# Optimization experiments

Hardware: AMD Instinct MI355X
Metric: run time of the kernel (lower is better)

The kernel has to match this reference:

```python
import jax, jax.numpy as jnp
import numpy as np

N = 100000      # nodes
E = 1600000     # directed edges (avg degree 16)
DIN, DH, DOUT = 128, 128, 64


def gcn_conv(x, W, b, src, dst, n):
    """PyG GCNConv: out = D^{-1/2} (A + I) D^{-1/2} (x @ W) + b.
    src/dst already include self-loops."""
    deg = jax.ops.segment_sum(jnp.ones_like(src, dtype=x.dtype), dst, num_segments=n)
    dinv = jnp.where(deg > 0, jax.lax.rsqrt(deg), jnp.zeros_like(deg))
    norm = dinv[src] * dinv[dst]                      # [E+N]
    h = x @ W                                         # [N, dout] linear first (PyG)
    msg = h[src] * norm[:, None]                      # gather + scale, [E+N, dout]
    return jax.ops.segment_sum(msg, dst, num_segments=n) + b


def setup_inputs() -> dict:
    key = jax.random.key(0)
    k1, k2, k3 = jax.random.split(key, 3)
    x = jax.random.normal(k1, (N, DIN), dtype=jnp.float32)
    edge_index = jax.random.randint(k2, (2, E), 0, N, dtype=jnp.int64)
    kw1, kw2 = jax.random.split(k3)
    # glorot-style init for the two GCN linear weights
    W1 = jax.random.normal(kw1, (DIN, DH), dtype=jnp.float32) * (1.0 / np.sqrt(DIN))
    b1 = jnp.zeros((DH,), dtype=jnp.float32)
    W2 = jax.random.normal(kw2, (DH, DOUT), dtype=jnp.float32) * (1.0 / np.sqrt(DH))
    b2 = jnp.zeros((DOUT,), dtype=jnp.float32)
    return {"x": x, "W1": W1, "b1": b1, "W2": W2, "b2": b2, "edge_index": edge_index}


def reference(x, W1, b1, W2, b2, edge_index):
    n = x.shape[0]
    loops = jnp.arange(n, dtype=edge_index.dtype)
    src = jnp.concatenate([edge_index[0], loops])     # add self-loops
    dst = jnp.concatenate([edge_index[1], loops])
    h = jax.nn.relu(gcn_conv(x, W1, b1, src, dst, n))
    return gcn_conv(h, W2, b2, src, dst, n)
```

## Files before the change

### kernel.cpp

```cpp
#include <hip/hip_runtime.h>

#define N_NODES 100000
#define N_EDGES 1600000
#define BUCKET_SHIFT 9
#define NB 196
#define BIN_BLOCKS 782
#define GEMM_BLOCKS 1563
#define BCAP 10240
#define AGG1_BLOCKS 6250
#define AGG2_BLOCKS 3125

typedef short bf16x8 __attribute__((ext_vector_type(8)));
typedef float f32x4 __attribute__((ext_vector_type(4)));
typedef float f32x8 __attribute__((ext_vector_type(8)));

__device__ __forceinline__ unsigned short f2bf(float f) {
    unsigned int u = __float_as_uint(f);
    unsigned int r = (u + 0x7FFFu + ((u >> 16) & 1u)) >> 16;
    return (unsigned short)r;
}
__device__ __forceinline__ float bf2f(unsigned short b) {
    return __uint_as_float(((unsigned int)b) << 16);
}
__device__ __forceinline__ void acc8(float* a, uint4 v) {
    a[0] += __uint_as_float(v.x << 16);
    a[1] += __uint_as_float(v.x & 0xFFFF0000u);
    a[2] += __uint_as_float(v.y << 16);
    a[3] += __uint_as_float(v.y & 0xFFFF0000u);
    a[4] += __uint_as_float(v.z << 16);
    a[5] += __uint_as_float(v.z & 0xFFFF0000u);
    a[6] += __uint_as_float(v.w << 16);
    a[7] += __uint_as_float(v.w & 0xFFFF0000u);
}

__global__ __launch_bounds__(256) void k_tw(const float* __restrict__ W1, const float* __restrict__ W2,
                                            unsigned short* __restrict__ w1t, unsigned short* __restrict__ w2t,
                                            int* __restrict__ bcur) {
    int t = blockIdx.x * 256 + threadIdx.x;
    if (t < 16384) {
        int k = t >> 7, c = t & 127;
        w1t[c * 128 + k] = f2bf(W1[t]);
    } else if (t < 24576) {
        int i = t - 16384;
        int k = i >> 6, c = i & 63;
        w2t[c * 128 + k] = f2bf(W2[i]);
    } else if (t - 24576 < NB) {
        bcur[t - 24576] = 0;
    }
}

__global__ __launch_bounds__(256) void k_bin(const int* __restrict__ src, const int* __restrict__ dst,
                                             int* __restrict__ bcur, int* __restrict__ ebuf) {
    __shared__ int hist[NB];
    __shared__ int lbase[NB];
    int t = threadIdx.x;
    int e0 = blockIdx.x * 2048 + t;
    int s[8], d[8];
#pragma unroll
    for (int j = 0; j < 8; ++j) {
        int e = e0 + j * 256;
        bool ok = e < N_EDGES;
        s[j] = ok ? src[e] : -1;
        d[j] = ok ? dst[e] : 0;
    }
    if (t < NB) hist[t] = 0;
    __syncthreads();
#pragma unroll
    for (int j = 0; j < 8; ++j)
        if (s[j] >= 0) atomicAdd(&hist[d[j] >> BUCKET_SHIFT], 1);
    __syncthreads();
    if (t < NB && hist[t] > 0) lbase[t] = atomicAdd(&bcur[t], hist[t]);
    __syncthreads();
    if (t < NB) hist[t] = 0;
    __syncthreads();
#pragma unroll
    for (int j = 0; j < 8; ++j) {
        if (s[j] >= 0) {
            int b = d[j] >> BUCKET_SHIFT;
            int r = lbase[b] + atomicAdd(&hist[b], 1);
            if (r < BCAP) ebuf[b * BCAP + r] = ((d[j] & 511) << 17) | s[j];
        }
    }
}

__global__ __launch_bounds__(256) void k_bfill3(const int* __restrict__ ebuf, const int* __restrict__ bcur,
                                                int* __restrict__ rowptr, float* __restrict__ dinv,
                                                int* __restrict__ csr) {
    __shared__ int sc[256];
    __shared__ int cnt[512];
    __shared__ int cur[512];
    int b = blockIdx.x, t = threadIdx.x;
    int node0 = b << BUCKET_SHIFT;
    int v = (t < NB) ? bcur[t] : 0;
    sc[t] = v;
    cnt[t] = 0;
    cnt[t + 256] = 0;
    __syncthreads();
    for (int off = 1; off < 256; off <<= 1) {
        int u = (t >= off) ? sc[t - off] : 0;
        __syncthreads();
        sc[t] += u;
        __syncthreads();
    }
    int cb = bcur[b];
    int s0 = sc[b] - cb;
    int ctot = cb > BCAP ? BCAP : cb;
    const int* eb = ebuf + b * BCAP;
    for (int i = t; i < ctot; i += 256) atomicAdd(&cnt[eb[i] >> 17], 1);
    __syncthreads();
    int c0 = cnt[2 * t], c1 = cnt[2 * t + 1];
    int ps = c0 + c1;
    sc[t] = ps;
    __syncthreads();
    for (int off = 1; off < 256; off <<= 1) {
        int u = (t >= off) ? sc[t - off] : 0;
        __syncthreads();
        sc[t] += u;
        __syncthreads();
    }
    int e0x = sc[t] - ps;
    int p0 = s0 + e0x, p1 = s0 + e0x + c0;
    int n0 = node0 + 2 * t, n1 = n0 + 1;
    if (n0 < N_NODES) { rowptr[n0] = p0; dinv[n0] = rsqrtf(1.0f + (float)c0); }
    if (n1 < N_NODES) { rowptr[n1] = p1; dinv[n1] = rsqrtf(1.0f + (float)c1); }
    if (b == NB - 1 && t == 0) rowptr[N_NODES] = N_EDGES;
    cur[2 * t] = p0;
    cur[2 * t + 1] = p1;
    __syncthreads();
    for (int i = t; i < ctot; i += 256) {
        int e = eb[i];
        int p = atomicAdd(&cur[e >> 17], 1);
        csr[p] = e & 0x1FFFF;
    }
}

__global__ __launch_bounds__(256) void k_gemm1(const float* __restrict__ x, const unsigned short* __restrict__ w1t,
                                               const float* __restrict__ dinv, unsigned short* __restrict__ hsb) {
    __shared__ unsigned short Xl[64 * 136];
    __shared__ unsigned short Wl[128 * 136];
    int t = threadIdx.x;
    int row0 = blockIdx.x * 64;
    for (int i = t; i < 64 * 32; i += 256) {
        int r = i >> 5, c4 = i & 31;
        int row = row0 + r;
        float4 v = (row < N_NODES) ? ((const float4*)x)[(long long)row * 32 + c4]
                                   : make_float4(0.f, 0.f, 0.f, 0.f);
        ushort4 o;
        o.x = f2bf(v.x); o.y = f2bf(v.y); o.z = f2bf(v.z); o.w = f2bf(v.w);
        *(ushort4*)&Xl[r * 136 + c4 * 4] = o;
    }
    for (int i = t; i < 128 * 16; i += 256) {
        int r = i >> 4, c8 = i & 15;
        *(bf16x8*)&Wl[r * 136 + c8 * 8] = *(const bf16x8*)&w1t[r * 128 + c8 * 8];
    }
    __syncthreads();
    int w = t >> 6, lane = t & 63;
    int nn = lane & 15, quad = lane >> 4;
    bf16x8 a[4];
#pragma unroll
    for (int kt = 0; kt < 4; ++kt)
        a[kt] = *(const bf16x8*)&Xl[(w * 16 + nn) * 136 + kt * 32 + quad * 8];
    f32x4 acc[8];
#pragma unroll
    for (int ct = 0; ct < 8; ++ct) {
        acc[ct] = (f32x4){0.f, 0.f, 0.f, 0.f};
#pragma unroll
        for (int kt = 0; kt < 4; ++kt) {
            bf16x8 b = *(const bf16x8*)&Wl[(ct * 16 + nn) * 136 + kt * 32 + quad * 8];
            acc[ct] = __builtin_amdgcn_mfma_f32_16x16x32_bf16(a[kt], b, acc[ct], 0, 0, 0);
        }
    }
#pragma unroll
    for (int r = 0; r < 4; ++r) {
        int row = row0 + w * 16 + quad * 4 + r;
        float dv = (row < N_NODES) ? dinv[row] : 0.f;
#pragma unroll
        for (int ct = 0; ct < 8; ++ct)
            Xl[(w * 16 + quad * 4 + r) * 136 + ct * 16 + nn] = f2bf(acc[ct][r] * dv);
    }
#pragma unroll
    for (int j = 0; j < 8; ++j) {
        int c = lane + j * 64;
        int r = c >> 5, c4 = c & 31;
        int row = row0 + w * 16 + r;
        if (row < N_NODES)
            ((ushort4*)(hsb + (long long)row * 128))[c4] = *(const ushort4*)&Xl[(w * 16 + r) * 136 + c4 * 4];
    }
}

__global__ __launch_bounds__(256) void k_agg1(const unsigned short* __restrict__ hsb, const int* __restrict__ rowptr,
                                              const int* __restrict__ csr, const float* __restrict__ dinv,
                                              const float* __restrict__ b1, unsigned short* __restrict__ h) {
    unsigned g = (blockIdx.x * 256 + threadIdx.x) >> 4;
    unsigned li = threadIdx.x & 15;
    if (g >= N_NODES) return;
    unsigned co = li * 8;
    float a[8];
    {
        uint4 sv = *(const uint4*)(hsb + (g << 7) + co);
        a[0] = __uint_as_float(sv.x << 16);
        a[1] = __uint_as_float(sv.x & 0xFFFF0000u);
        a[2] = __uint_as_float(sv.y << 16);
        a[3] = __uint_as_float(sv.y & 0xFFFF0000u);
        a[4] = __uint_as_float(sv.z << 16);
        a[5] = __uint_as_float(sv.z & 0xFFFF0000u);
        a[6] = __uint_as_float(sv.w << 16);
        a[7] = __uint_as_float(sv.w & 0xFFFF0000u);
    }
    int k = rowptr[g], end = rowptr[g + 1];
    for (; k + 7 < end; k += 8) {
        int i0 = csr[k + 0], i1 = csr[k + 1], i2 = csr[k + 2], i3 = csr[k + 3];
        int i4 = csr[k + 4], i5 = csr[k + 5], i6 = csr[k + 6], i7 = csr[k + 7];
        uint4 v0 = *(const uint4*)(hsb + (((unsigned)i0) << 7) + co);
        uint4 v1 = *(const uint4*)(hsb + (((unsigned)i1) << 7) + co);
        uint4 v2 = *(const uint4*)(hsb + (((unsigned)i2) << 7) + co);
        uint4 v3 = *(const uint4*)(hsb + (((unsigned)i3) << 7) + co);
        uint4 v4 = *(const uint4*)(hsb + (((unsigned)i4) << 7) + co);
        uint4 v5 = *(const uint4*)(hsb + (((unsigned)i5) << 7) + co);
        uint4 v6 = *(const uint4*)(hsb + (((unsigned)i6) << 7) + co);
        uint4 v7 = *(const uint4*)(hsb + (((unsigned)i7) << 7) + co);
        acc8(a, v0); acc8(a, v1); acc8(a, v2); acc8(a, v3);
        acc8(a, v4); acc8(a, v5); acc8(a, v6); acc8(a, v7);
    }
    if (k + 3 < end) {
        int i0 = csr[k + 0], i1 = csr[k + 1], i2 = csr[k + 2], i3 = csr[k + 3];
        uint4 v0 = *(const uint4*)(hsb + (((unsigned)i0) << 7) + co);
        uint4 v1 = *(const uint4*)(hsb + (((unsigned)i1) << 7) + co);
        uint4 v2 = *(const uint4*)(hsb + (((unsigned)i2) << 7) + co);
        uint4 v3 = *(const uint4*)(hsb + (((unsigned)i3) << 7) + co);
        acc8(a, v0); acc8(a, v1); acc8(a, v2); acc8(a, v3);
        k += 4;
    }
    for (; k < end; ++k) {
        uint4 v = *(const uint4*)(hsb + (((unsigned)csr[k]) << 7) + co);
        acc8(a, v);
    }
    float dv = dinv[g];
    f32x8 bb = *(const f32x8*)(b1 + li * 8);
    bf16x8 o;
#pragma unroll
    for (int j = 0; j < 8; ++j)
        o[j] = (short)f2bf(fmaxf(fmaf(dv, a[j], bb[j]), 0.f));
    *(bf16x8*)(h + (g << 7) + co) = o;
}

__global__ __launch_bounds__(256) void k_gemm2(const unsigned short* __restrict__ h, const unsigned short* __restrict__ w2t,
                                               const float* __restrict__ dinv, unsigned short* __restrict__ gsb) {
    __shared__ unsigned short Hl[64 * 136];
    __shared__ unsigned short Wl[64 * 136];
    int t = threadIdx.x;
    int row0 = blockIdx.x * 64;
    for (int i = t; i < 64 * 16; i += 256) {
        int r = i >> 4, c8 = i & 15;
        int row = row0 + r;
        bf16x8 v = (row < N_NODES) ? *(const bf16x8*)&h[(long long)row * 128 + c8 * 8]
                                   : (bf16x8){0, 0, 0, 0, 0, 0, 0, 0};
        *(bf16x8*)&Hl[r * 136 + c8 * 8] = v;
        *(bf16x8*)&Wl[r * 136 + c8 * 8] = *(const bf16x8*)&w2t[r * 128 + c8 * 8];
    }
    __syncthreads();
    int w = t >> 6, lane = t & 63;
    int nn = lane & 15, quad = lane >> 4;
    bf16x8 a[4];
#pragma unroll
    for (int kt = 0; kt < 4; ++kt)
        a[kt] = *(const bf16x8*)&Hl[(w * 16 + nn) * 136 + kt * 32 + quad * 8];
    f32x4 acc[4];
#pragma unroll
    for (int ct = 0; ct < 4; ++ct) {
        acc[ct] = (f32x4){0.f, 0.f, 0.f, 0.f};
#pragma unroll
        for (int kt = 0; kt < 4; ++kt) {
            bf16x8 b = *(const bf16x8*)&Wl[(ct * 16 + nn) * 136 + kt * 32 + quad * 8];
            acc[ct] = __builtin_amdgcn_mfma_f32_16x16x32_bf16(a[kt], b, acc[ct], 0, 0, 0);
        }
    }
#pragma unroll
    for (int r = 0; r < 4; ++r) {
        int row = row0 + w * 16 + quad * 4 + r;
        float dv = (row < N_NODES) ? dinv[row] : 0.f;
#pragma unroll
        for (int ct = 0; ct < 4; ++ct)
            Hl[(w * 16 + quad * 4 + r) * 136 + ct * 16 + nn] = f2bf(acc[ct][r] * dv);
    }
#pragma unroll
    for (int j = 0; j < 4; ++j) {
        int c = lane + j * 64;
        int r = c >> 4, c4 = c & 15;
        int row = row0 + w * 16 + r;
        if (row < N_NODES)
            ((ushort4*)(gsb + (long long)row * 64))[c4] = *(const ushort4*)&Hl[(w * 16 + r) * 136 + c4 * 4];
    }
}

__global__ __launch_bounds__(256) void k_agg2(const unsigned short* __restrict__ gsb, const int* __restrict__ rowptr,
                                              const int* __restrict__ csr, const float* __restrict__ dinv,
                                              const float* __restrict__ b2, float* __restrict__ out) {
    unsigned g = (blockIdx.x * 256 + threadIdx.x) >> 3;
    unsigned li = threadIdx.x & 7;
    if (g >= N_NODES) return;
    unsigned co = li * 8;
    float a[8];
    {
        uint4 sv = *(const uint4*)(gsb + (g << 6) + co);
        a[0] = __uint_as_float(sv.x << 16);
        a[1] = __uint_as_float(sv.x & 0xFFFF0000u);
        a[2] = __uint_as_float(sv.y << 16);
        a[3] = __uint_as_float(sv.y & 0xFFFF0000u);
        a[4] = __uint_as_float(sv.z << 16);
        a[5] = __uint_as_float(sv.z & 0xFFFF0000u);
        a[6] = __uint_as_float(sv.w << 16);
        a[7] = __uint_as_float(sv.w & 0xFFFF0000u);
    }
    int k = rowptr[g], end = rowptr[g + 1];
    for (; k + 7 < end; k += 8) {
        int i0 = csr[k + 0], i1 = csr[k + 1], i2 = csr[k + 2], i3 = csr[k + 3];
        int i4 = csr[k + 4], i5 = csr[k + 5], i6 = csr[k + 6], i7 = csr[k + 7];
        uint4 v0 = *(const uint4*)(gsb + (((unsigned)i0) << 6) + co);
        uint4 v1 = *(const uint4*)(gsb + (((unsigned)i1) << 6) + co);
        uint4 v2 = *(const uint4*)(gsb + (((unsigned)i2) << 6) + co);
        uint4 v3 = *(const uint4*)(gsb + (((unsigned)i3) << 6) + co);
        uint4 v4 = *(const uint4*)(gsb + (((unsigned)i4) << 6) + co);
        uint4 v5 = *(const uint4*)(gsb + (((unsigned)i5) << 6) + co);
        uint4 v6 = *(const uint4*)(gsb + (((unsigned)i6) << 6) + co);
        uint4 v7 = *(const uint4*)(gsb + (((unsigned)i7) << 6) + co);
        acc8(a, v0); acc8(a, v1); acc8(a, v2); acc8(a, v3);
        acc8(a, v4); acc8(a, v5); acc8(a, v6); acc8(a, v7);
    }
    if (k + 3 < end) {
        int i0 = csr[k + 0], i1 = csr[k + 1], i2 = csr[k + 2], i3 = csr[k + 3];
        uint4 v0 = *(const uint4*)(gsb + (((unsigned)i0) << 6) + co);
        uint4 v1 = *(const uint4*)(gsb + (((unsigned)i1) << 6) + co);
        uint4 v2 = *(const uint4*)(gsb + (((unsigned)i2) << 6) + co);
        uint4 v3 = *(const uint4*)(gsb + (((unsigned)i3) << 6) + co);
        acc8(a, v0); acc8(a, v1); acc8(a, v2); acc8(a, v3);
        k += 4;
    }
    for (; k < end; ++k) {
        uint4 v = *(const uint4*)(gsb + (((unsigned)csr[k]) << 6) + co);
        acc8(a, v);
    }
    float dv = dinv[g];
    f32x8 bb = *(const f32x8*)(b2 + li * 8);
    float4 o0 = make_float4(fmaf(dv, a[0], bb[0]), fmaf(dv, a[1], bb[1]),
                            fmaf(dv, a[2], bb[2]), fmaf(dv, a[3], bb[3]));
    float4 o1 = make_float4(fmaf(dv, a[4], bb[4]), fmaf(dv, a[5], bb[5]),
                            fmaf(dv, a[6], bb[6]), fmaf(dv, a[7], bb[7]));
    float* op = out + ((long long)g << 6) + co;
    *(float4*)op = o0;
    *(float4*)(op + 4) = o1;
}

extern "C" void kernel_launch(void* const* d_in, const int* in_sizes, int n_in,
                              void* d_out, int out_size, void* d_ws, size_t ws_size,
                              hipStream_t stream) {
    const float* x  = (const float*)d_in[0];
    const float* W1 = (const float*)d_in[1];
    const float* b1 = (const float*)d_in[2];
    const float* W2 = (const float*)d_in[3];
    const float* b2 = (const float*)d_in[4];
    const int*   ei = (const int*)d_in[5];
    const int* src = ei;
    const int* dst = ei + N_EDGES;
    float* out = (float*)d_out;

    char* ws = (char*)d_ws;
    int*   csr    = (int*)(ws + 0);
    int*   rowptr = (int*)(ws + 6800000);
    float* dinv   = (float*)(ws + 7200256);
    int*   bcur   = (int*)(ws + 7604352);
    unsigned short* w1t = (unsigned short*)(ws + 7608448);
    unsigned short* w2t = (unsigned short*)(ws + 7641216);
    int*   ebuf   = (int*)(ws + 8388608);
    unsigned short* hsb = (unsigned short*)(ws + 8388608);
    unsigned short* h   = (unsigned short*)(ws + 59588608);
    unsigned short* gsb = hsb;

    k_tw<<<97, 256, 0, stream>>>(W1, W2, w1t, w2t, bcur);
    k_bin<<<BIN_BLOCKS, 256, 0, stream>>>(src, dst, bcur, ebuf);
    k_bfill3<<<NB, 256, 0, stream>>>(ebuf, bcur, rowptr, dinv, csr);

    k_gemm1<<<GEMM_BLOCKS, 256, 0, stream>>>(x, w1t, dinv, hsb);
    k_agg1<<<AGG1_BLOCKS, 256, 0, stream>>>(hsb, rowptr, csr, dinv, b1, h);
    k_gemm2<<<GEMM_BLOCKS, 256, 0, stream>>>(h, w2t, dinv, gsb);
    k_agg2<<<AGG2_BLOCKS, 256, 0, stream>>>(gsb, rowptr, csr, dinv, b2, out);
}
```

Measured before the change: 269.1 us.

## Fuse layer-1 aggregation with layer-2 GEMM in one 1024-thread kernel

Layer-1 neighbor aggregation and the layer-2 GEMM now run in one kernel. Each 1024-thread block aggregates 64 nodes into shared memory, then applies W2 with MFMA and writes the dinv-scaled result straight to gsb. This removes the write and re-read of the 128-wide intermediate h and one kernel launch. In exchange, the GEMM phase waits on the slowest node's gather in each block, and the large blocks may limit occupancy and latency hiding for the irregular gathers.

Measured after the change: 276.2 us. 2.6% more time.

```diff
diff --git a/kernel.cpp b/kernel.cpp
--- a/kernel.cpp
+++ b/kernel.cpp
@@ -7,7 +7,6 @@
 #define BIN_BLOCKS 782
 #define GEMM_BLOCKS 1563
 #define BCAP 10240
-#define AGG1_BLOCKS 6250
 #define AGG2_BLOCKS 3125
 
 typedef short bf16x8 __attribute__((ext_vector_type(8)));
@@ -188,108 +187,103 @@
     }
 }
 
-__global__ __launch_bounds__(256) void k_agg1(const unsigned short* __restrict__ hsb, const int* __restrict__ rowptr,
-                                              const int* __restrict__ csr, const float* __restrict__ dinv,
-                                              const float* __restrict__ b1, unsigned short* __restrict__ h) {
-    unsigned g = (blockIdx.x * 256 + threadIdx.x) >> 4;
-    unsigned li = threadIdx.x & 15;
-    if (g >= N_NODES) return;
-    unsigned co = li * 8;
-    float a[8];
-    {
-        uint4 sv = *(const uint4*)(hsb + (g << 7) + co);
-        a[0] = __uint_as_float(sv.x << 16);
-        a[1] = __uint_as_float(sv.x & 0xFFFF0000u);
-        a[2] = __uint_as_float(sv.y << 16);
-        a[3] = __uint_as_float(sv.y & 0xFFFF0000u);
-        a[4] = __uint_as_float(sv.z << 16);
-        a[5] = __uint_as_float(sv.z & 0xFFFF0000u);
-        a[6] = __uint_as_float(sv.w << 16);
-        a[7] = __uint_as_float(sv.w & 0xFFFF0000u);
-    }
-    int k = rowptr[g], end = rowptr[g + 1];
-    for (; k + 7 < end; k += 8) {
-        int i0 = csr[k + 0], i1 = csr[k + 1], i2 = csr[k + 2], i3 = csr[k + 3];
-        int i4 = csr[k + 4], i5 = csr[k + 5], i6 = csr[k + 6], i7 = csr[k + 7];
-        uint4 v0 = *(const uint4*)(hsb + (((unsigned)i0) << 7) + co);
-        uint4 v1 = *(const uint4*)(hsb + (((unsigned)i1) << 7) + co);
-        uint4 v2 = *(const uint4*)(hsb + (((unsigned)i2) << 7) + co);
-        uint4 v3 = *(const uint4*)(hsb + (((unsigned)i3) << 7) + co);
-        uint4 v4 = *(const uint4*)(hsb + (((unsigned)i4) << 7) + co);
-        uint4 v5 = *(const uint4*)(hsb + (((unsigned)i5) << 7) + co);
-        uint4 v6 = *(const uint4*)(hsb + (((unsigned)i6) << 7) + co);
-        uint4 v7 = *(const uint4*)(hsb + (((unsigned)i7) << 7) + co);
-        acc8(a, v0); acc8(a, v1); acc8(a, v2); acc8(a, v3);
-        acc8(a, v4); acc8(a, v5); acc8(a, v6); acc8(a, v7);
-    }
-    if (k + 3 < end) {
-        int i0 = csr[k + 0], i1 = csr[k + 1], i2 = csr[k + 2], i3 = csr[k + 3];
-        uint4 v0 = *(const uint4*)(hsb + (((unsigned)i0) << 7) + co);
-        uint4 v1 = *(const uint4*)(hsb + (((unsigned)i1) << 7) + co);
-        uint4 v2 = *(const uint4*)(hsb + (((unsigned)i2) << 7) + co);
-        uint4 v3 = *(const uint4*)(hsb + (((unsigned)i3) << 7) + co);
-        acc8(a, v0); acc8(a, v1); acc8(a, v2); acc8(a, v3);
-        k += 4;
-    }
-    for (; k < end; ++k) {
-        uint4 v = *(const uint4*)(hsb + (((unsigned)csr[k]) << 7) + co);
-        acc8(a, v);
-    }
-    float dv = dinv[g];
-    f32x8 bb = *(const f32x8*)(b1 + li * 8);
-    bf16x8 o;
-#pragma unroll
-    for (int j = 0; j < 8; ++j)
-        o[j] = (short)f2bf(fmaxf(fmaf(dv, a[j], bb[j]), 0.f));
-    *(bf16x8*)(h + (g << 7) + co) = o;
-}
-
-__global__ __launch_bounds__(256) void k_gemm2(const unsigned short* __restrict__ h, const unsigned short* __restrict__ w2t,
-                                               const float* __restrict__ dinv, unsigned short* __restrict__ gsb) {
+__global__ __launch_bounds__(1024) void k_agg1g2(const unsigned short* __restrict__ hsb, const int* __restrict__ rowptr,
+                                                 const int* __restrict__ csr, const float* __restrict__ dinv,
+                                                 const float* __restrict__ b1, const unsigned short* __restrict__ w2t,
+                                                 unsigned short* __restrict__ gsb) {
     __shared__ unsigned short Hl[64 * 136];
     __shared__ unsigned short Wl[64 * 136];
     int t = threadIdx.x;
     int row0 = blockIdx.x * 64;
-    for (int i = t; i < 64 * 16; i += 256) {
-        int r = i >> 4, c8 = i & 15;
+
+    {
+        int r = t >> 4, c8 = t & 15;
+        *(bf16x8*)&Wl[r * 136 + c8 * 8] = *(const bf16x8*)&w2t[r * 128 + c8 * 8];
+    }
+
+    int gl = t >> 4;
+    unsigned li = t & 15;
+    unsigned g = (unsigned)(row0 + gl);
+    unsigned co = li * 8;
+    bool valid = g < N_NODES;
+    if (valid) {
+        float a[8];
+        {
+            uint4 sv = *(const uint4*)(hsb + ((long long)g << 7) + co);
+            a[0] = __uint_as_float(sv.x << 16);
+            a[1] = __uint_as_float(sv.x & 0xFFFF0000u);
+            a[2] = __uint_as_float(sv.y << 16);
+            a[3] = __uint_as_float(sv.y & 0xFFFF0000u);
+            a[4] = __uint_as_float(sv.z << 16);
+            a[5] = __uint_as_float(sv.z & 0xFFFF0000u);
+            a[6] = __uint_as_float(sv.w << 16);
+            a[7] = __uint_as_float(sv.w & 0xFFFF0000u);
+        }
+        int k = rowptr[g], end = rowptr[g + 1];
+        for (; k + 7 < end; k += 8) {
+            int i0 = csr[k + 0], i1 = csr[k + 1], i2 = csr[k + 2], i3 = csr[k + 3];
+            int i4 = csr[k + 4], i5 = csr[k + 5], i6 = csr[k + 6], i7 = csr[k + 7];
+            uint4 v0 = *(const uint4*)(hsb + (((unsigned)i0) << 7) + co);
+            uint4 v1 = *(const uint4*)(hsb + (((unsigned)i1) << 7) + co);
+            uint4 v2 = *(const uint4*)(hsb + (((unsigned)i2) << 7) + co);
+            uint4 v3 = *(const uint4*)(hsb + (((unsigned)i3) << 7) + co);
+            uint4 v4 = *(const uint4*)(hsb + (((unsigned)i4) << 7) + co);
+            uint4 v5 = *(const uint4*)(hsb + (((unsigned)i5) << 7) + co);
+            uint4 v6 = *(const uint4*)(hsb + (((unsigned)i6) << 7) + co);
+            uint4 v7 = *(const uint4*)(hsb + (((unsigned)i7) << 7) + co);
+            acc8(a, v0); acc8(a, v1); acc8(a, v2); acc8(a, v3);
+            acc8(a, v4); acc8(a, v5); acc8(a, v6); acc8(a, v7);
+        }
+        if (k + 3 < end) {
+            int i0 = csr[k + 0], i1 = csr[k + 1], i2 = csr[k + 2], i3 = csr[k + 3];
+            uint4 v0 = *(const uint4*)(hsb + (((unsigned)i0) << 7) + co);
+            uint4 v1 = *(const uint4*)(hsb + (((unsigned)i1) << 7) + co);
+            uint4 v2 = *(const uint4*)(hsb + (((unsigned)i2) << 7) + co);
+            uint4 v3 = *(const uint4*)(hsb + (((unsigned)i3) << 7) + co);
+            acc8(a, v0); acc8(a, v1); acc8(a, v2); acc8(a, v3);
+            k += 4;
+        }
+        for (; k < end; ++k) {
+            uint4 v = *(const uint4*)(hsb + (((unsigned)csr[k]) << 7) + co);
+            acc8(a, v);
+        }
+        float dv = dinv[g];
+        f32x8 bb = *(const f32x8*)(b1 + li * 8);
+        bf16x8 o;
+#pragma unroll
+        for (int j = 0; j < 8; ++j)
+            o[j] = (short)f2bf(fmaxf(fmaf(dv, a[j], bb[j]), 0.f));
+        *(bf16x8*)&Hl[gl * 136 + co] = o;
+    }
+    __syncthreads();
+
+    int w = t >> 6, lane = t & 63;
+    int rt = w >> 2, ctile = w & 3;
+    int nn = lane & 15, quad = lane >> 4;
+    bf16x8 af[4];
+#pragma unroll
+    for (int kt = 0; kt < 4; ++kt)
+        af[kt] = *(const bf16x8*)&Hl[(rt * 16 + nn) * 136 + kt * 32 + quad * 8];
+    f32x4 acc = (f32x4){0.f, 0.f, 0.f, 0.f};
+#pragma unroll
+    for (int kt = 0; kt < 4; ++kt) {
+        bf16x8 bfr = *(const bf16x8*)&Wl[(ctile * 16 + nn) * 136 + kt * 32 + quad * 8];
+        acc = __builtin_amdgcn_mfma_f32_16x16x32_bf16(af[kt], bfr, acc, 0, 0, 0);
+    }
+    __syncthreads();
+#pragma unroll
+    for (int r = 0; r < 4; ++r) {
+        int rl = rt * 16 + quad * 4 + r;
+        int row = row0 + rl;
+        float dv = (row < N_NODES) ? dinv[row] : 0.f;
+        Hl[rl * 136 + ctile * 16 + nn] = f2bf(acc[r] * dv);
+    }
+    __syncthreads();
+    {
+        int r = t >> 4, c4 = t & 15;
         int row = row0 + r;
-        bf16x8 v = (row < N_NODES) ? *(const bf16x8*)&h[(long long)row * 128 + c8 * 8]
-                                   : (bf16x8){0, 0, 0, 0, 0, 0, 0, 0};
-        *(bf16x8*)&Hl[r * 136 + c8 * 8] = v;
-        *(bf16x8*)&Wl[r * 136 + c8 * 8] = *(const bf16x8*)&w2t[r * 128 + c8 * 8];
-    }
-    __syncthreads();
-    int w = t >> 6, lane = t & 63;
-    int nn = lane & 15, quad = lane >> 4;
-    bf16x8 a[4];
-#pragma unroll
-    for (int kt = 0; kt < 4; ++kt)
-        a[kt] = *(const bf16x8*)&Hl[(w * 16 + nn) * 136 + kt * 32 + quad * 8];
-    f32x4 acc[4];
-#pragma unroll
-    for (int ct = 0; ct < 4; ++ct) {
-        acc[ct] = (f32x4){0.f, 0.f, 0.f, 0.f};
-#pragma unroll
-        for (int kt = 0; kt < 4; ++kt) {
-            bf16x8 b = *(const bf16x8*)&Wl[(ct * 16 + nn) * 136 + kt * 32 + quad * 8];
-            acc[ct] = __builtin_amdgcn_mfma_f32_16x16x32_bf16(a[kt], b, acc[ct], 0, 0, 0);
-        }
-    }
-#pragma unroll
-    for (int r = 0; r < 4; ++r) {
-        int row = row0 + w * 16 + quad * 4 + r;
-        float dv = (row < N_NODES) ? dinv[row] : 0.f;
-#pragma unroll
-        for (int ct = 0; ct < 4; ++ct)
-            Hl[(w * 16 + quad * 4 + r) * 136 + ct * 16 + nn] = f2bf(acc[ct][r] * dv);
-    }
-#pragma unroll
-    for (int j = 0; j < 4; ++j) {
-        int c = lane + j * 64;
-        int r = c >> 4, c4 = c & 15;
-        int row = row0 + w * 16 + r;
         if (row < N_NODES)
-            ((ushort4*)(gsb + (long long)row * 64))[c4] = *(const ushort4*)&Hl[(w * 16 + r) * 136 + c4 * 4];
+            ((ushort4*)(gsb + (long long)row * 64))[c4] = *(const ushort4*)&Hl[r * 136 + c4 * 4];
     }
 }
 
@@ -373,15 +367,13 @@
     unsigned short* w2t = (unsigned short*)(ws + 7641216);
     int*   ebuf   = (int*)(ws + 8388608);
     unsigned short* hsb = (unsigned short*)(ws + 8388608);
-    unsigned short* h   = (unsigned short*)(ws + 59588608);
-    unsigned short* gsb = hsb;
+    unsigned short* gsb = (unsigned short*)(ws + 59588608);
 
     k_tw<<<97, 256, 0, stream>>>(W1, W2, w1t, w2t, bcur);
     k_bin<<<BIN_BLOCKS, 256, 0, stream>>>(src, dst, bcur, ebuf);
     k_bfill3<<<NB, 256, 0, stream>>>(ebuf, bcur, rowptr, dinv, csr);
 
     k_gemm1<<<GEMM_BLOCKS, 256, 0, stream>>>(x, w1t, dinv, hsb);
-    k_agg1<<<AGG1_BLOCKS, 256, 0, stream>>>(hsb, rowptr, csr, dinv, b1, h);
-    k_gemm2<<<GEMM_BLOCKS, 256, 0, stream>>>(h, w2t, dinv, gsb);
+    k_agg1g2<<<GEMM_BLOCKS, 1024, 0, stream>>>(hsb, rowptr, csr, dinv, b1, w2t, gsb);
     k_agg2<<<AGG2_BLOCKS, 256, 0, stream>>>(gsb, rowptr, csr, dinv, b2, out);
 }
```

## Use finer CSR buckets and move bucket prefix scan to separate kernel

Applied to the files above, without the earlier changes.

Shrinks the CSR-build buckets from 512 to 128 destination nodes, giving 782 buckets instead of 196 so the fill kernel runs more blocks and spreads work across more CUs. The global prefix scan over bucket counts is split out into a single-block kernel instead of being recomputed by every fill block. The per-bucket scan now covers 128 slots. This adds one kernel launch, a much larger shared histogram and more global atomics in the binning pass, and a tighter per-bucket capacity that could overflow on skewed graphs.

Result: no change. 271.7 us (+1.0%).

```diff
diff --git a/kernel.cpp b/kernel.cpp
--- a/kernel.cpp
+++ b/kernel.cpp
@@ -2,11 +2,11 @@
 
 #define N_NODES 100000
 #define N_EDGES 1600000
-#define BUCKET_SHIFT 9
-#define NB 196
+#define BUCKET_SHIFT 7
+#define NB 782
 #define BIN_BLOCKS 782
 #define GEMM_BLOCKS 1563
-#define BCAP 10240
+#define BCAP 2816
 #define AGG1_BLOCKS 6250
 #define AGG2_BLOCKS 3125
 
@@ -63,69 +63,76 @@
         s[j] = ok ? src[e] : -1;
         d[j] = ok ? dst[e] : 0;
     }
-    if (t < NB) hist[t] = 0;
+    for (int i = t; i < NB; i += 256) hist[i] = 0;
     __syncthreads();
 #pragma unroll
     for (int j = 0; j < 8; ++j)
         if (s[j] >= 0) atomicAdd(&hist[d[j] >> BUCKET_SHIFT], 1);
     __syncthreads();
-    if (t < NB && hist[t] > 0) lbase[t] = atomicAdd(&bcur[t], hist[t]);
-    __syncthreads();
-    if (t < NB) hist[t] = 0;
+    for (int i = t; i < NB; i += 256)
+        if (hist[i] > 0) lbase[i] = atomicAdd(&bcur[i], hist[i]);
+    __syncthreads();
+    for (int i = t; i < NB; i += 256) hist[i] = 0;
     __syncthreads();
 #pragma unroll
     for (int j = 0; j < 8; ++j) {
         if (s[j] >= 0) {
             int b = d[j] >> BUCKET_SHIFT;
             int r = lbase[b] + atomicAdd(&hist[b], 1);
-            if (r < BCAP) ebuf[b * BCAP + r] = ((d[j] & 511) << 17) | s[j];
+            if (r < BCAP) ebuf[b * BCAP + r] = ((d[j] & 127) << 17) | s[j];
         }
     }
 }
 
-__global__ __launch_bounds__(256) void k_bfill3(const int* __restrict__ ebuf, const int* __restrict__ bcur,
-                                                int* __restrict__ rowptr, float* __restrict__ dinv,
-                                                int* __restrict__ csr) {
-    __shared__ int sc[256];
-    __shared__ int cnt[512];
-    __shared__ int cur[512];
-    int b = blockIdx.x, t = threadIdx.x;
-    int node0 = b << BUCKET_SHIFT;
+__global__ __launch_bounds__(1024) void k_scan(const int* __restrict__ bcur, int* __restrict__ bbase,
+                                               int* __restrict__ rowptr) {
+    __shared__ int sc[1024];
+    int t = threadIdx.x;
     int v = (t < NB) ? bcur[t] : 0;
     sc[t] = v;
-    cnt[t] = 0;
-    cnt[t + 256] = 0;
-    __syncthreads();
-    for (int off = 1; off < 256; off <<= 1) {
+    __syncthreads();
+    for (int off = 1; off < 1024; off <<= 1) {
         int u = (t >= off) ? sc[t - off] : 0;
         __syncthreads();
         sc[t] += u;
         __syncthreads();
     }
+    if (t < NB) bbase[t] = sc[t] - v;
+    if (t == 0) rowptr[N_NODES] = N_EDGES;
+}
+
+__global__ __launch_bounds__(256) void k_bfill3(const int* __restrict__ ebuf, const int* __restrict__ bcur,
+                                                const int* __restrict__ bbase,
+                                                int* __restrict__ rowptr, float* __restrict__ dinv,
+                                                int* __restrict__ csr) {
+    __shared__ int cnt[128];
+    __shared__ int sc[128];
+    __shared__ int cur[128];
+    int b = blockIdx.x, t = threadIdx.x;
+    int node0 = b << BUCKET_SHIFT;
+    if (t < 128) cnt[t] = 0;
     int cb = bcur[b];
-    int s0 = sc[b] - cb;
+    int s0 = bbase[b];
     int ctot = cb > BCAP ? BCAP : cb;
     const int* eb = ebuf + b * BCAP;
+    __syncthreads();
     for (int i = t; i < ctot; i += 256) atomicAdd(&cnt[eb[i] >> 17], 1);
     __syncthreads();
-    int c0 = cnt[2 * t], c1 = cnt[2 * t + 1];
-    int ps = c0 + c1;
-    sc[t] = ps;
-    __syncthreads();
-    for (int off = 1; off < 256; off <<= 1) {
-        int u = (t >= off) ? sc[t - off] : 0;
+    int c = (t < 128) ? cnt[t] : 0;
+    if (t < 128) sc[t] = c;
+    __syncthreads();
+    for (int off = 1; off < 128; off <<= 1) {
+        int u = (t < 128 && t >= off) ? sc[t - off] : 0;
         __syncthreads();
-        sc[t] += u;
+        if (t < 128) sc[t] += u;
         __syncthreads();
     }
-    int e0x = sc[t] - ps;
-    int p0 = s0 + e0x, p1 = s0 + e0x + c0;
-    int n0 = node0 + 2 * t, n1 = n0 + 1;
-    if (n0 < N_NODES) { rowptr[n0] = p0; dinv[n0] = rsqrtf(1.0f + (float)c0); }
-    if (n1 < N_NODES) { rowptr[n1] = p1; dinv[n1] = rsqrtf(1.0f + (float)c1); }
-    if (b == NB - 1 && t == 0) rowptr[N_NODES] = N_EDGES;
-    cur[2 * t] = p0;
-    cur[2 * t + 1] = p1;
+    if (t < 128) {
+        int p = s0 + sc[t] - c;
+        int n = node0 + t;
+        if (n < N_NODES) { rowptr[n] = p; dinv[n] = rsqrtf(1.0f + (float)c); }
+        cur[t] = p;
+    }
     __syncthreads();
     for (int i = t; i < ctot; i += 256) {
         int e = eb[i];
@@ -371,14 +378,16 @@
     int*   bcur   = (int*)(ws + 7604352);
     unsigned short* w1t = (unsigned short*)(ws + 7608448);
     unsigned short* w2t = (unsigned short*)(ws + 7641216);
+    int*   bbase  = (int*)(ws + 7657600);
     int*   ebuf   = (int*)(ws + 8388608);
     unsigned short* hsb = (unsigned short*)(ws + 8388608);
     unsigned short* h   = (unsigned short*)(ws + 59588608);
     unsigned short* gsb = hsb;
 
-    k_tw<<<97, 256, 0, stream>>>(W1, W2, w1t, w2t, bcur);
+    k_tw<<<100, 256, 0, stream>>>(W1, W2, w1t, w2t, bcur);
     k_bin<<<BIN_BLOCKS, 256, 0, stream>>>(src, dst, bcur, ebuf);
-    k_bfill3<<<NB, 256, 0, stream>>>(ebuf, bcur, rowptr, dinv, csr);
+    k_scan<<<1, 1024, 0, stream>>>(bcur, bbase, rowptr);
+    k_bfill3<<<NB, 256, 0, stream>>>(ebuf, bcur, bbase, rowptr, dinv, csr);
 
     k_gemm1<<<GEMM_BLOCKS, 256, 0, stream>>>(x, w1t, dinv, hsb);
     k_agg1<<<AGG1_BLOCKS, 256, 0, stream>>>(hsb, rowptr, csr, dinv, b1, h);
```
